# Kernel optimization log

Hardware: AMD Instinct MI355X
Metric: run time of the kernel (lower is better)

The kernel has to match this reference:

```python
import jax, jax.numpy as jnp
import numpy as np

B, C, H, T, K = 32, 128, 512, 8192, 512


def setup_inputs() -> dict:
    key = jax.random.key(0)
    ks = jax.random.split(key, 4)
    s = 0.02
    return {
        "x": jax.random.normal(ks[0], (B, C, T), dtype=jnp.float32),
        "up_w": jax.random.normal(ks[1], (H, C), dtype=jnp.float32) * s,
        "up_b": jnp.zeros((H,), jnp.float32),
        "sal_w": jax.random.normal(ks[2], (H, C), dtype=jnp.float32) * s,
        "sal_b": jnp.zeros((H,), jnp.float32),
        "down_w": jax.random.normal(ks[3], (C, H), dtype=jnp.float32) * s,
        "down_b": jnp.zeros((C,), jnp.float32),
        "k_sparse": K,
    }


def reference(x, up_w, up_b, sal_w, sal_b, down_w, down_b, k_sparse):
    b = x.shape[0]
    # 1x1 Conv1d == per-timestep GEMM
    sig = jnp.einsum('bct,hc->bht', x, up_w) + up_b[None, :, None]   # [B,H,T]
    sal = jnp.einsum('bct,hc->bht', x, sal_w) + sal_b[None, :, None]  # [B,H,T]
    # global softmax over flattened (H*T) per batch item
    flat = jax.nn.softmax(sal.reshape(b, -1), axis=-1)                # [B,H*T]
    # k-sparse: keep top-k values, zero everything else
    vals, idx = jax.lax.top_k(flat, k_sparse)                          # [B,K]
    sparse = jnp.zeros_like(flat).at[jnp.arange(b)[:, None], idx].set(vals)
    sal_sparse = sparse.reshape(sig.shape)                             # [B,H,T]
    gated = sig * sal_sparse                                           # [B,H,T]
    out = jnp.einsum('bht,ch->bct', gated, down_w) + down_b[None, :, None]
    return out
```

## Files before the change

### kernel.cpp

```cpp
#include <hip/hip_runtime.h>
#include <hip/hip_bf16.h>
#include <math.h>

#define BB 32
#define CC 128
#define HH 512
#define TT 8192
#define KMAX 512

#define NBIN 2048
#define CANDCAP 4096
#define HOTCAP 32768
#define TILES 2048
#define TLCAP 256
#define HFLOOR 0.6f
#define BW (0.875f / 2048.0f)
#define INVBW (2048.0f / 0.875f)
#define DELTA_C2 6e-3f
#define DELTA_C1 1.2e-2f

#define N_HIST 0
#define N_SUMEXP 262144
#define N_CANDCNT 262400
#define N_TILECNT 262528
#define N_ZERO 270720
#define N_TAU 270848
#define N_SELCNT 270976
#define N_CELLMAX 271360
#define N_TLIST 8659968
#define N_CANDVAL 10757120
#define N_CANDIDX 11805696
#define N_SELIDX 12329984
#define N_SELVAL 12395520
#define N_SWB 12461056
#define N_XF 12592128
#define N_DWT 79700992
#define N_NEED 79963136

#define O_HIST 0
#define O_SUMEXP 262144
#define O_CANDCNT 262400
#define O_HOTCNT 262528
#define O_ZERO 262656
#define O_TAU 262656
#define O_SELCNT 262784
#define O_CELLMAX 263168
#define O_HOTLIST 8651776
#define O_CANDVAL 8782848
#define O_CANDIDX 9831424
#define O_SELIDX 10355712
#define O_SELVAL 10421248

typedef __attribute__((ext_vector_type(8))) short short8;
typedef __attribute__((ext_vector_type(16))) float f32x16;
typedef __attribute__((address_space(3))) unsigned int lds_u32;
typedef const __attribute__((address_space(1))) unsigned int glb_u32;


__global__ void prep_w(const float* __restrict__ sw, short* __restrict__ swb) {
  int i = blockIdx.x * 256 + threadIdx.x;
  int m = i & 31, u = (i >> 5) & 1, kc = (i >> 6) & 7, w = (i >> 9) & 3, by = i >> 11;
  int h = by * 128 + w * 32 + m;
  int c0 = kc * 16 + u * 8;
  float4 f0 = *(const float4*)(sw + (size_t)h * CC + c0);
  float4 f1 = *(const float4*)(sw + (size_t)h * CC + c0 + 4);
  union { __hip_bfloat162 h2; unsigned u; } p0, p1, p2, p3;
  p0.h2 = __float22bfloat162_rn(make_float2(f0.x, f0.y));
  p1.h2 = __float22bfloat162_rn(make_float2(f0.z, f0.w));
  p2.h2 = __float22bfloat162_rn(make_float2(f1.x, f1.y));
  p3.h2 = __float22bfloat162_rn(make_float2(f1.z, f1.w));
  *(uint4*)(swb + (size_t)i * 8) = make_uint4(p0.u, p1.u, p2.u, p3.u);
}

__global__ void prep_dwt(const float* __restrict__ dw, float* __restrict__ dwt) {
  int i = blockIdx.x * 256 + threadIdx.x;
  int c = i & 127, h = i >> 7;
  dwt[(size_t)h * CC + c] = dw[(size_t)c * HH + h];
}

__global__ __launch_bounds__(256) void prep_xt(const float* __restrict__ x,
                                               short* __restrict__ xf) {
  __shared__ float Lt[128 * 128];
  int tid = threadIdx.x;
  int b = blockIdx.y, bx = blockIdx.x, t0g = bx * 128;
  const float* xb = x + (size_t)b * CC * TT;
  {
    int cq = tid >> 5, tq = tid & 31, t0 = tq * 4;
#pragma unroll
    for (int p = 0; p < 4; p++) {
      int c0 = p * 32 + cq * 4;
      float r0[4], r1[4], r2[4], r3[4];
      *(float4*)r0 = *(const float4*)(xb + (size_t)(c0 + 0) * TT + t0g + t0);
      *(float4*)r1 = *(const float4*)(xb + (size_t)(c0 + 1) * TT + t0g + t0);
      *(float4*)r2 = *(const float4*)(xb + (size_t)(c0 + 2) * TT + t0g + t0);
      *(float4*)r3 = *(const float4*)(xb + (size_t)(c0 + 3) * TT + t0g + t0);
#pragma unroll
      for (int j = 0; j < 4; j++) {
        int t = t0 + j;
        int addr = t * 128 + ((((c0 >> 2) ^ (t & 31)) << 2));
        *(float4*)&Lt[addr] = make_float4(r0[j], r1[j], r2[j], r3[j]);
      }
    }
  }
  __syncthreads();
  int u = tid & 1, m = (tid >> 1) & 31, nt = (tid >> 6) & 3;
  int t = nt * 32 + m;
  short* dst = xf + ((size_t)b * 64 + bx) * 16384 + nt * 4096 + u * 256 + m * 8;
#pragma unroll
  for (int kc = 0; kc < 8; kc++) {
    int c0 = kc * 16 + u * 8;
    float4 f0 = *(float4*)&Lt[t * 128 + ((((c0 >> 2) ^ (t & 31)) << 2))];
    float4 f1 = *(float4*)&Lt[t * 128 + (((((c0 + 4) >> 2) ^ (t & 31)) << 2))];
    union { __hip_bfloat162 h2; unsigned u; } p0, p1, p2, p3;
    p0.h2 = __float22bfloat162_rn(make_float2(f0.x, f0.y));
    p1.h2 = __float22bfloat162_rn(make_float2(f0.z, f0.w));
    p2.h2 = __float22bfloat162_rn(make_float2(f1.x, f1.y));
    p3.h2 = __float22bfloat162_rn(make_float2(f1.z, f1.w));
    *(uint4*)(dst + kc * 512) = make_uint4(p0.u, p1.u, p2.u, p3.u);
  }
}

__global__ __launch_bounds__(256) void pass_a_lds(const short* __restrict__ xf,
                                                  const short* __restrict__ swb,
                                                  const float* __restrict__ sb,
                                                  float* __restrict__ cellmax,
                                                  int* __restrict__ hist,
                                                  double* __restrict__ sumexp) {
  __shared__ short Xs[16384];
  __shared__ double sered[4];
  int tid = threadIdx.x;
  int w = tid >> 6, lane = tid & 63, m = lane & 31, u = lane >> 5;
  int id = blockIdx.x, b = blockIdx.y;
  int bx = ((id >> 5) << 3) | (id & 7);
  int by = (id >> 3) & 3;

  const short* xsl = xf + ((size_t)b * 64 + bx) * 16384;
  {
    const short* gs = xsl + w * 4096 + lane * 8;
    short* ls = &Xs[w * 4096];
#pragma unroll
    for (int i = 0; i < 8; i++) {
      __builtin_amdgcn_global_load_lds((glb_u32*)(gs + i * 512),
                                       (lds_u32*)(ls + i * 512), 16, 0, 0);
    }
  }

  const short* wb_ = swb + (size_t)(by * 4 + w) * 4096 + u * 256 + m * 8;
  short8 afr[8];
#pragma unroll
  for (int kc = 0; kc < 8; kc++) afr[kc] = *(const short8*)(wb_ + kc * 512);

  __syncthreads();

  f32x16 acc0, acc1, acc2, acc3;
#pragma unroll
  for (int r = 0; r < 16; r++) { acc0[r] = 0.f; acc1[r] = 0.f; acc2[r] = 0.f; acc3[r] = 0.f; }

  const short* xr = &Xs[u * 256 + m * 8];
#pragma unroll
  for (int kc = 0; kc < 8; kc++) {
    short8 b0 = *(const short8*)(xr + kc * 512);
    short8 b1 = *(const short8*)(xr + 4096 + kc * 512);
    short8 b2 = *(const short8*)(xr + 8192 + kc * 512);
    short8 b3 = *(const short8*)(xr + 12288 + kc * 512);
    acc0 = __builtin_amdgcn_mfma_f32_32x32x16_bf16(afr[kc], b0, acc0, 0, 0, 0);
    acc1 = __builtin_amdgcn_mfma_f32_32x32x16_bf16(afr[kc], b1, acc1, 0, 0, 0);
    acc2 = __builtin_amdgcn_mfma_f32_32x32x16_bf16(afr[kc], b2, acc2, 0, 0, 0);
    acc3 = __builtin_amdgcn_mfma_f32_32x32x16_bf16(afr[kc], b3, acc3, 0, 0, 0);
  }

  int h0 = by * 128;
  float tmax = -1e30f;
  float se = 0.f;
#define EPI(ACC)                                                              \
  {                                                                           \
    _Pragma("unroll") for (int g = 0; g < 4; g++) {                           \
      float bias4[4];                                                         \
      *(float4*)bias4 = *(const float4*)&sb[h0 + w * 32 + g * 8 + u * 4];     \
      _Pragma("unroll") for (int q = 0; q < 4; q++) {                         \
        float s = ACC[g * 4 + q] + bias4[q];                                  \
        tmax = fmaxf(tmax, s);                                                \
        se += __expf(s);                                                      \
        if (s >= HFLOOR) {                                                    \
          int bin = (int)((s - HFLOOR) * INVBW);                              \
          if (bin > NBIN - 1) bin = NBIN - 1;                                 \
          atomicAdd(&hist[b * NBIN + bin], 1);                                \
        }                                                                     \
      }                                                                       \
    }                                                                         \
  }
  EPI(acc0) EPI(acc1) EPI(acc2) EPI(acc3)
#undef EPI
  int cid = ((b * 4 + by) * 64 + bx) * 256 + tid;
  cellmax[cid] = tmax;
  double sed = (double)se;
#pragma unroll
  for (int mm = 1; mm < 64; mm <<= 1) sed += __shfl_xor(sed, mm);
  if (lane == 0) sered[w] = sed;
  __syncthreads();
  if (tid == 0) atomicAdd(&sumexp[b], sered[0] + sered[1] + sered[2] + sered[3]);
}

__global__ void pass_b(const int* __restrict__ hist, float* __restrict__ tau,
                       const int* __restrict__ kptr) {
  __shared__ int hsh[NBIN];
  __shared__ int ps[256];
  int b = blockIdx.x, tid = threadIdx.x;
  int part = 0;
#pragma unroll
  for (int j = 0; j < 8; j++) {
    int v = hist[b * NBIN + tid * 8 + j];
    hsh[tid * 8 + j] = v;
    part += v;
  }
  ps[tid] = part;
  __syncthreads();
  if (tid == 0) {
    int k = kptr[0];
    if (k < 1) k = 1;
    if (k > KMAX) k = KMAX;
    long cum = 0;
    float tv = HFLOOR;
    for (int i = 255; i >= 0; i--) {
      if (cum + ps[i] >= k) {
        long r = k - cum;
        long c2 = 0;
        for (int j = 7; j >= 0; j--) {
          c2 += hsh[i * 8 + j];
          if (c2 >= r) { tv = HFLOOR + (i * 8 + j) * BW; break; }
        }
        break;
      }
      cum += ps[i];
    }
    tau[b] = tv;
  }
}

__global__ void pass_c1_fast(const float* __restrict__ cellmax, const float* __restrict__ tau,
                             int* __restrict__ tilecnt, int* __restrict__ tlist) {
  int i = blockIdx.x * blockDim.x + threadIdx.x;
  float v = cellmax[i];
  int b = i >> 16;
  if (v >= tau[b] - DELTA_C1) {
    int tile = (b << 6) | ((i >> 8) & 63);
    int pos = atomicAdd(&tilecnt[tile], 1);
    if (pos < TLCAP) tlist[tile * TLCAP + pos] = i;
  }
}

__global__ __launch_bounds__(256) void pass_c2_fast(
    const float* __restrict__ x, const float* __restrict__ sw,
    const float* __restrict__ sb, const float* __restrict__ tau,
    const int* __restrict__ tilecnt, const int* __restrict__ tlist,
    int* __restrict__ candcnt, double* __restrict__ candval, int* __restrict__ candidx) {
  __shared__ float Xt[128 * 132];
  int tile = blockIdx.x;
  int b = tile >> 6, bx = tile & 63;
  int cnt = tilecnt[tile];
  if (cnt <= 0) return;
  if (cnt > TLCAP) cnt = TLCAP;
  int tid = threadIdx.x;
  {
    int cq = tid >> 5, tq = tid & 31;
    int t4 = tq * 4, snt = t4 >> 5, sa = (t4 >> 2) & 7;
    int sdst = snt * 32 + (((sa + snt) & 7) << 2);
    const float* xb = x + (size_t)b * CC * TT + bx * 128;
#pragma unroll
    for (int p = 0; p < 16; p++) {
      int c = p * 8 + cq;
      *(float4*)&Xt[c * 132 + sdst] = *(const float4*)(xb + (size_t)c * TT + t4);
    }
  }
  __syncthreads();
  int wv = tid >> 6, lane = tid & 63;
  float tmb = tau[b] - DELTA_C2;
  for (int s = wv; s < cnt; s += 4) {
    int cid = tlist[tile * TLCAP + s];
    int by = (cid >> 14) & 3;
    int ta = cid & 255;
    int w = ta >> 6, lc = ta & 63, m = lc & 31, u = lc >> 5;
    int nt = lane >> 4, r = lane & 15;
    int h = by * 128 + w * 32 + (r >> 2) * 8 + (r & 3) + 4 * u;
    int t = bx * 128 + nt * 32 + m;
    const float* swr = sw + (size_t)h * CC;
    int xoff = nt * 32 + (((((m >> 2) + nt) & 7)) << 2) + (m & 3);
    double a0 = 0.0, a1 = 0.0;
#pragma unroll 4
    for (int c = 0; c < CC; c += 2) {
      a0 = fma((double)Xt[c * 132 + xoff], (double)swr[c], a0);
      a1 = fma((double)Xt[(c + 1) * 132 + xoff], (double)swr[c + 1], a1);
    }
    double acc = a0 + a1 + (double)sb[h];
    if (acc >= (double)tmb) {
      int pos = atomicAdd(&candcnt[b], 1);
      if (pos < CANDCAP) {
        candval[b * CANDCAP + pos] = acc;
        candidx[b * CANDCAP + pos] = h * TT + t;
      }
    }
  }
}

__global__ void pass_d(const int* __restrict__ candcnt, const double* __restrict__ candval,
                       const int* __restrict__ candidx, const double* __restrict__ sumexp,
                       const int* __restrict__ kptr, int* __restrict__ selidx,
                       float* __restrict__ selval, int* __restrict__ selcnt) {
  __shared__ double sv[CANDCAP];
  __shared__ int si[CANDCAP];
  int b = blockIdx.x;
  int n = candcnt[b];
  if (n > CANDCAP) n = CANDCAP;
  int k = kptr[0];
  if (k < 0) k = 0;
  if (k > KMAX) k = KMAX;
  for (int i = threadIdx.x; i < n; i += blockDim.x) {
    sv[i] = candval[b * CANDCAP + i];
    si[i] = candidx[b * CANDCAP + i];
  }
  __syncthreads();
  double S = sumexp[b];
  for (int i = threadIdx.x; i < n; i += blockDim.x) {
    double vi = sv[i];
    int ii = si[i];
    int rank = 0;
    for (int q = 0; q < n; q++) {
      double vq = sv[q];
      rank += (vq > vi) || (vq == vi && si[q] < ii);
    }
    if (rank < k) {
      selidx[b * KMAX + rank] = ii;
      selval[b * KMAX + rank] = (float)(exp(vi) / S);
    }
  }
  if (threadIdx.x == 0) selcnt[b] = n < k ? n : k;
}

__global__ void pass_e1(const float* __restrict__ db, float* __restrict__ out) {
  int row = blockIdx.x;
  int c = row & (CC - 1);
  float v = db[c];
  float4 v4 = make_float4(v, v, v, v);
  float4* o = (float4*)(out + (size_t)row * TT);
#pragma unroll
  for (int q = 0; q < 8; q++) o[q * 256 + threadIdx.x] = v4;
}

__global__ void pass_e2_fast(const short* __restrict__ xf, const float* __restrict__ uw,
                             const float* __restrict__ ub, const float* __restrict__ dwt,
                             const int* __restrict__ selidx, const float* __restrict__ selval,
                             const int* __restrict__ selcnt, float* __restrict__ out) {
  int b = blockIdx.y, j = blockIdx.x;
  if (j >= selcnt[b]) return;
  int idx = selidx[b * KMAX + j];
  float val = selval[b * KMAX + j];
  int h = idx >> 13, t = idx & (TT - 1);
  int bx = t >> 7, tl = t & 127, nt = tl >> 5, m = tl & 31;
  int lane = threadIdx.x;
  const short* xt = xf + ((size_t)b * 64 + bx) * 16384 + nt * 4096 + m * 8;
  int off = (lane >> 3) * 512 + ((lane >> 2) & 1) * 256 + (lane & 3) * 2;
  __hip_bfloat162 hv = *(const __hip_bfloat162*)(xt + off);
  float2 xv = __bfloat1622float2(hv);
  int c0 = lane * 2;
  float2 wv = *(const float2*)(uw + (size_t)h * CC + c0);
  float p = xv.x * wv.x + xv.y * wv.y;
#pragma unroll
  for (int mm = 1; mm < 64; mm <<= 1) p += __shfl_xor(p, mm);
  float sig = p + ub[h];
  float g = sig * val;
  float2 dv = *(const float2*)(dwt + (size_t)h * CC + c0);
  atomicAdd(&out[((size_t)b * CC + c0) * TT + t], g * dv.x);
  atomicAdd(&out[((size_t)b * CC + c0 + 1) * TT + t], g * dv.y);
}

__global__ __launch_bounds__(256) void pass_a_slow(const float* __restrict__ x,
                                                   const float* __restrict__ sw,
                                                   const float* __restrict__ sb,
                                                   float* __restrict__ cellmax,
                                                   int* __restrict__ hist,
                                                   double* __restrict__ sumexp) {
  __shared__ short Ws[128 * 128];
  __shared__ short Xs[128 * 128];
  __shared__ float sbs[128];
  int tid = threadIdx.x;
  int b = blockIdx.z, by = blockIdx.y, bx = blockIdx.x;
  int h0 = by * 128, t0g = bx * 128;
  const float* xb = x + (size_t)b * CC * TT;
  {
    int cq = tid >> 5, tq = tid & 31;
    int t0 = tq * 4;
#pragma unroll
    for (int p = 0; p < 4; p++) {
      int c0 = p * 32 + cq * 4;
      float r0[4], r1[4], r2[4], r3[4];
      *(float4*)r0 = *(const float4*)(xb + (size_t)(c0 + 0) * TT + t0g + t0);
      *(float4*)r1 = *(const float4*)(xb + (size_t)(c0 + 1) * TT + t0g + t0);
      *(float4*)r2 = *(const float4*)(xb + (size_t)(c0 + 2) * TT + t0g + t0);
      *(float4*)r3 = *(const float4*)(xb + (size_t)(c0 + 3) * TT + t0g + t0);
#pragma unroll
      for (int j = 0; j < 4; j++) {
        int t = t0 + j;
        int addr = t * 128 + ((((c0 >> 3) ^ (t & 15)) << 3) | (c0 & 7));
        union { __hip_bfloat162 h; unsigned int u; } a0, a1;
        a0.h = __float22bfloat162_rn(make_float2(r0[j], r1[j]));
        a1.h = __float22bfloat162_rn(make_float2(r2[j], r3[j]));
        *(uint2*)&Xs[addr] = make_uint2(a0.u, a1.u);
      }
    }
  }
  {
    int hh = tid >> 1, c4 = (tid & 1) << 2;
#pragma unroll
    for (int k = 0; k < 16; k++) {
      int c0 = k * 8 + c4;
      float r[4];
      *(float4*)r = *(const float4*)(sw + (size_t)(h0 + hh) * CC + c0);
      int addr = hh * 128 + ((((c0 >> 3) ^ (hh & 15)) << 3) | (c0 & 7));
      union { __hip_bfloat162 h; unsigned int u; } a0, a1;
      a0.h = __float22bfloat162_rn(make_float2(r[0], r[1]));
      a1.h = __float22bfloat162_rn(make_float2(r[2], r[3]));
      *(uint2*)&Ws[addr] = make_uint2(a0.u, a1.u);
    }
  }
  if (tid < 128) sbs[tid] = sb[h0 + tid];
  __syncthreads();
  int w = tid >> 6, lane = tid & 63, m = lane & 31, u = lane >> 5;
  f32x16 acc0, acc1, acc2, acc3;
#pragma unroll
  for (int r = 0; r < 16; r++) { acc0[r] = 0.f; acc1[r] = 0.f; acc2[r] = 0.f; acc3[r] = 0.f; }
  const short* wrow = &Ws[(w * 32 + m) * 128];
  const short* xrow = &Xs[m * 128];
#pragma unroll
  for (int kc = 0; kc < 8; kc++) {
    int pc = ((((kc << 1) | u) ^ (m & 15)) << 3);
    short8 af = *(const short8*)(wrow + pc);
    short8 b0 = *(const short8*)(xrow + 0 * 32 * 128 + pc);
    short8 b1 = *(const short8*)(xrow + 1 * 32 * 128 + pc);
    short8 b2 = *(const short8*)(xrow + 2 * 32 * 128 + pc);
    short8 b3 = *(const short8*)(xrow + 3 * 32 * 128 + pc);
    acc0 = __builtin_amdgcn_mfma_f32_32x32x16_bf16(af, b0, acc0, 0, 0, 0);
    acc1 = __builtin_amdgcn_mfma_f32_32x32x16_bf16(af, b1, acc1, 0, 0, 0);
    acc2 = __builtin_amdgcn_mfma_f32_32x32x16_bf16(af, b2, acc2, 0, 0, 0);
    acc3 = __builtin_amdgcn_mfma_f32_32x32x16_bf16(af, b3, acc3, 0, 0, 0);
  }
  float tmax = -1e30f;
  float se = 0.f;
#define EPI(ACC)                                                              \
  {                                                                           \
    _Pragma("unroll") for (int g = 0; g < 4; g++) {                           \
      float bias4[4];                                                         \
      *(float4*)bias4 = *(float4*)&sbs[w * 32 + g * 8 + u * 4];               \
      _Pragma("unroll") for (int q = 0; q < 4; q++) {                         \
        float s = ACC[g * 4 + q] + bias4[q];                                  \
        tmax = fmaxf(tmax, s);                                                \
        se += __expf(s);                                                      \
        if (s >= HFLOOR) {                                                    \
          int bin = (int)((s - HFLOOR) * INVBW);                              \
          if (bin > NBIN - 1) bin = NBIN - 1;                                 \
          atomicAdd(&hist[b * NBIN + bin], 1);                                \
        }                                                                     \
      }                                                                       \
    }                                                                         \
  }
  EPI(acc0) EPI(acc1) EPI(acc2) EPI(acc3)
#undef EPI
  int cid = ((b * 4 + by) * 64 + bx) * 256 + tid;
  cellmax[cid] = tmax;
  double sed = (double)se;
#pragma unroll
  for (int mm = 1; mm < 64; mm <<= 1) sed += __shfl_xor(sed, mm);
  if ((tid & 63) == 0) atomicAdd(&sumexp[b], sed);
}

__global__ void pass_c1_slow(const float* __restrict__ cellmax, const float* __restrict__ tau,
                             int* __restrict__ hotcnt, int* __restrict__ hotlist) {
  int i = blockIdx.x * blockDim.x + threadIdx.x;
  float v = cellmax[i];
  int b = i >> 16;
  if (v >= tau[b] - DELTA_C1) {
    int pos = atomicAdd(hotcnt, 1);
    if (pos < HOTCAP) hotlist[pos] = i;
  }
}

__global__ void pass_c2_slow(const float* __restrict__ x, const float* __restrict__ sw,
                             const float* __restrict__ sb, const float* __restrict__ tau,
                             const int* __restrict__ hotcnt, const int* __restrict__ hotlist,
                             int* __restrict__ candcnt, double* __restrict__ candval,
                             int* __restrict__ candidx) {
  int j = blockIdx.x;
  int n = hotcnt[0];
  if (n > HOTCAP) n = HOTCAP;
  if (j >= n) return;
  int cid = hotlist[j];
  int b = cid >> 16, by = (cid >> 14) & 3, bx = (cid >> 8) & 63;
  int ta = cid & 255;
  int w = ta >> 6, lane = ta & 63, m = lane & 31, u = lane >> 5;
  int e = threadIdx.x;
  int nt = e >> 4, r = e & 15;
  int h = by * 128 + w * 32 + (r >> 2) * 8 + (r & 3) + 4 * u;
  int t = bx * 128 + nt * 32 + m;
  const float* xb = x + (size_t)b * CC * TT;
  double acc = 0.0;
#pragma unroll 8
  for (int c = 0; c < CC; c++)
    acc += (double)xb[(size_t)c * TT + t] * (double)sw[h * CC + c];
  acc += (double)sb[h];
  float tm = tau[b] - DELTA_C2;
  if (acc >= (double)tm) {
    int pos = atomicAdd(&candcnt[b], 1);
    if (pos < CANDCAP) {
      candval[b * CANDCAP + pos] = acc;
      candidx[b * CANDCAP + pos] = h * TT + t;
    }
  }
}

__global__ void pass_e2_slow(const float* __restrict__ x, const float* __restrict__ uw,
                             const float* __restrict__ ub, const float* __restrict__ dw,
                             const int* __restrict__ selidx, const float* __restrict__ selval,
                             const int* __restrict__ selcnt, float* __restrict__ out) {
  int b = blockIdx.y, j = blockIdx.x;
  if (j >= selcnt[b]) return;
  int idx = selidx[b * KMAX + j];
  float val = selval[b * KMAX + j];
  int h = idx >> 13, t = idx & (TT - 1);
  int c = threadIdx.x;
  const float* xb = x + (size_t)b * CC * TT;
  float p = xb[(size_t)c * TT + t] * uw[h * CC + c] +
            xb[(size_t)(c + 64) * TT + t] * uw[h * CC + c + 64];
#pragma unroll
  for (int m = 1; m < 64; m <<= 1) p += __shfl_xor(p, m);
  float sig = p + ub[h];
  float g = sig * val;
  atomicAdd(&out[((size_t)b * CC + c) * TT + t], g * dw[c * HH + h]);
  atomicAdd(&out[((size_t)b * CC + c + 64) * TT + t], g * dw[(c + 64) * HH + h]);
}

extern "C" void kernel_launch(void* const* d_in, const int* in_sizes, int n_in,
                              void* d_out, int out_size, void* d_ws, size_t ws_size,
                              hipStream_t stream) {
  const float* x = (const float*)d_in[0];
  const float* uw = (const float*)d_in[1];
  const float* ub = (const float*)d_in[2];
  const float* sw = (const float*)d_in[3];
  const float* sb = (const float*)d_in[4];
  const float* dw = (const float*)d_in[5];
  const float* db = (const float*)d_in[6];
  const int* kptr = (const int*)d_in[7];
  float* out = (float*)d_out;
  char* ws = (char*)d_ws;

  if (ws_size >= (size_t)N_NEED) {
    int* hist = (int*)(ws + N_HIST);
    double* sumexp = (double*)(ws + N_SUMEXP);
    int* candcnt = (int*)(ws + N_CANDCNT);
    int* tilecnt = (int*)(ws + N_TILECNT);
    float* tau = (float*)(ws + N_TAU);
    int* selcnt = (int*)(ws + N_SELCNT);
    float* cellmax = (float*)(ws + N_CELLMAX);
    int* tlist = (int*)(ws + N_TLIST);
    double* candval = (double*)(ws + N_CANDVAL);
    int* candidx = (int*)(ws + N_CANDIDX);
    int* selidx = (int*)(ws + N_SELIDX);
    float* selval = (float*)(ws + N_SELVAL);
    short* swb = (short*)(ws + N_SWB);
    short* xf = (short*)(ws + N_XF);
    float* dwt = (float*)(ws + N_DWT);

    (void)hipMemsetAsync(d_ws, 0, N_ZERO, stream);
    prep_w<<<32, 256, 0, stream>>>(sw, swb);
    prep_dwt<<<256, 256, 0, stream>>>(dw, dwt);
    prep_xt<<<dim3(64, 32), 256, 0, stream>>>(x, xf);
    pass_a_lds<<<dim3(256, 32), 256, 0, stream>>>(xf, swb, sb, cellmax, hist, sumexp);
    pass_b<<<32, 256, 0, stream>>>(hist, tau, kptr);
    pass_c1_fast<<<8192, 256, 0, stream>>>(cellmax, tau, tilecnt, tlist);
    pass_c2_fast<<<TILES, 256, 0, stream>>>(x, sw, sb, tau, tilecnt, tlist, candcnt,
                                            candval, candidx);
    pass_d<<<32, 256, 0, stream>>>(candcnt, candval, candidx, sumexp, kptr, selidx,
                                   selval, selcnt);
    pass_e1<<<BB * CC, 256, 0, stream>>>(db, out);
    pass_e2_fast<<<dim3(KMAX, BB), 64, 0, stream>>>(xf, uw, ub, dwt, selidx, selval,
                                                    selcnt, out);
  } else {
    int* hist = (int*)(ws + O_HIST);
    double* sumexp = (double*)(ws + O_SUMEXP);
    int* candcnt = (int*)(ws + O_CANDCNT);
    int* hotcnt = (int*)(ws + O_HOTCNT);
    float* tau = (float*)(ws + O_TAU);
    int* selcnt = (int*)(ws + O_SELCNT);
    float* cellmax = (float*)(ws + O_CELLMAX);
    int* hotlist = (int*)(ws + O_HOTLIST);
    double* candval = (double*)(ws + O_CANDVAL);
    int* candidx = (int*)(ws + O_CANDIDX);
    int* selidx = (int*)(ws + O_SELIDX);
    float* selval = (float*)(ws + O_SELVAL);

    (void)hipMemsetAsync(d_ws, 0, O_ZERO, stream);
    pass_a_slow<<<dim3(64, 4, 32), 256, 0, stream>>>(x, sw, sb, cellmax, hist, sumexp);
    pass_b<<<32, 256, 0, stream>>>(hist, tau, kptr);
    pass_c1_slow<<<8192, 256, 0, stream>>>(cellmax, tau, hotcnt, hotlist);
    pass_c2_slow<<<HOTCAP, 64, 0, stream>>>(x, sw, sb, tau, hotcnt, hotlist, candcnt,
                                            candval, candidx);
    pass_d<<<32, 256, 0, stream>>>(candcnt, candval, candidx, sumexp, kptr, selidx,
                                   selval, selcnt);
    pass_e1<<<BB * CC, 256, 0, stream>>>(db, out);
    pass_e2_slow<<<dim3(KMAX, BB), 64, 0, stream>>>(x, uw, ub, dw, selidx, selval,
                                                    selcnt, out);
  }
}
```

Measured before the change: 923.7 us.

## Transpose LDS tile in candidate rescoring kernel and use vectorized double-buffered loads

The candidate rescoring kernel now stores the x tile transposed in shared memory (time-major with XOR swizzle), so each lane reads contiguous float4 channel vectors instead of scalar strided values. Weight rows are read as float4 with a two-stage register double buffer, and the next candidate index is prefetched. Blocks double to 512 threads (8 waves) to process more candidates in parallel. The costs are scalar LDS stores during the transpose and higher register pressure from the buffers.

```diff
diff --git a/kernel.cpp b/kernel.cpp
--- a/kernel.cpp
+++ b/kernel.cpp
@@ -249,7 +249,7 @@
   }
 }
 
-__global__ __launch_bounds__(256) void pass_c2_fast(
+__global__ __launch_bounds__(512, 4) void pass_c2_fast(
     const float* __restrict__ x, const float* __restrict__ sw,
     const float* __restrict__ sb, const float* __restrict__ tau,
     const int* __restrict__ tilecnt, const int* __restrict__ tlist,
@@ -262,41 +262,71 @@
   if (cnt > TLCAP) cnt = TLCAP;
   int tid = threadIdx.x;
   {
-    int cq = tid >> 5, tq = tid & 31;
-    int t4 = tq * 4, snt = t4 >> 5, sa = (t4 >> 2) & 7;
-    int sdst = snt * 32 + (((sa + snt) & 7) << 2);
+    int cq = tid >> 5, tq = tid & 31, t4 = tq * 4;
     const float* xb = x + (size_t)b * CC * TT + bx * 128;
 #pragma unroll
-    for (int p = 0; p < 16; p++) {
-      int c = p * 8 + cq;
-      *(float4*)&Xt[c * 132 + sdst] = *(const float4*)(xb + (size_t)c * TT + t4);
+    for (int p = 0; p < 8; p++) {
+      int c = p * 16 + cq;
+      float4 v = *(const float4*)(xb + (size_t)c * TT + t4);
+      Xt[(t4 + 0) * 132 + (c ^ ((((t4 + 0) >> 2) & 7) << 2))] = v.x;
+      Xt[(t4 + 1) * 132 + (c ^ ((((t4 + 1) >> 2) & 7) << 2))] = v.y;
+      Xt[(t4 + 2) * 132 + (c ^ ((((t4 + 2) >> 2) & 7) << 2))] = v.z;
+      Xt[(t4 + 3) * 132 + (c ^ ((((t4 + 3) >> 2) & 7) << 2))] = v.w;
     }
   }
   __syncthreads();
   int wv = tid >> 6, lane = tid & 63;
   float tmb = tau[b] - DELTA_C2;
-  for (int s = wv; s < cnt; s += 4) {
-    int cid = tlist[tile * TLCAP + s];
-    int by = (cid >> 14) & 3;
-    int ta = cid & 255;
-    int w = ta >> 6, lc = ta & 63, m = lc & 31, u = lc >> 5;
-    int nt = lane >> 4, r = lane & 15;
-    int h = by * 128 + w * 32 + (r >> 2) * 8 + (r & 3) + 4 * u;
-    int t = bx * 128 + nt * 32 + m;
-    const float* swr = sw + (size_t)h * CC;
-    int xoff = nt * 32 + (((((m >> 2) + nt) & 7)) << 2) + (m & 3);
-    double a0 = 0.0, a1 = 0.0;
-#pragma unroll 4
-    for (int c = 0; c < CC; c += 2) {
-      a0 = fma((double)Xt[c * 132 + xoff], (double)swr[c], a0);
-      a1 = fma((double)Xt[(c + 1) * 132 + xoff], (double)swr[c + 1], a1);
-    }
-    double acc = a0 + a1 + (double)sb[h];
-    if (acc >= (double)tmb) {
-      int pos = atomicAdd(&candcnt[b], 1);
-      if (pos < CANDCAP) {
-        candval[b * CANDCAP + pos] = acc;
-        candidx[b * CANDCAP + pos] = h * TT + t;
+  if (wv >= cnt && wv >= 8) {}
+  int s = wv;
+  if (s < cnt) {
+    int cid_nxt = tlist[tile * TLCAP + s];
+    for (; s < cnt; s += 8) {
+      int cid = cid_nxt;
+      if (s + 8 < cnt) cid_nxt = tlist[tile * TLCAP + s + 8];
+      int by = (cid >> 14) & 3;
+      int ta = cid & 255;
+      int w = ta >> 6, lc = ta & 63, m = lc & 31, u = lc >> 5;
+      int nt = lane >> 4, r = lane & 15;
+      int h = by * 128 + w * 32 + (r >> 2) * 8 + (r & 3) + 4 * u;
+      int t = bx * 128 + nt * 32 + m;
+      float sbh = sb[h];
+      const float4* swr = (const float4*)(sw + (size_t)h * CC);
+      const float* xrow = &Xt[(nt * 32 + m) * 132];
+      int swz = ((m >> 2) & 7) << 2;
+      double acc0 = 0.0, acc1 = 0.0;
+      float4 wbuf[2][4], xbuf[2][4];
+#pragma unroll
+      for (int j = 0; j < 4; j++) {
+        wbuf[0][j] = swr[j];
+        xbuf[0][j] = *(const float4*)(xrow + ((j * 4) ^ swz));
+      }
+#pragma unroll
+      for (int ch = 0; ch < 8; ch++) {
+        int cur = ch & 1, nxt = cur ^ 1;
+        if (ch < 7) {
+#pragma unroll
+          for (int j = 0; j < 4; j++) {
+            wbuf[nxt][j] = swr[(ch + 1) * 4 + j];
+            xbuf[nxt][j] = *(const float4*)(xrow + (((ch + 1) * 16 + j * 4) ^ swz));
+          }
+        }
+#pragma unroll
+        for (int j = 0; j < 4; j++) {
+          float4 wvv = wbuf[cur][j], xvv = xbuf[cur][j];
+          acc0 = fma((double)xvv.x, (double)wvv.x, acc0);
+          acc1 = fma((double)xvv.y, (double)wvv.y, acc1);
+          acc0 = fma((double)xvv.z, (double)wvv.z, acc0);
+          acc1 = fma((double)xvv.w, (double)wvv.w, acc1);
+        }
+      }
+      double acc = acc0 + acc1 + (double)sbh;
+      if (acc >= (double)tmb) {
+        int pos = atomicAdd(&candcnt[b], 1);
+        if (pos < CANDCAP) {
+          candval[b * CANDCAP + pos] = acc;
+          candidx[b * CANDCAP + pos] = h * TT + t;
+        }
       }
     }
   }
@@ -575,7 +605,7 @@
     pass_a_lds<<<dim3(256, 32), 256, 0, stream>>>(xf, swb, sb, cellmax, hist, sumexp);
     pass_b<<<32, 256, 0, stream>>>(hist, tau, kptr);
     pass_c1_fast<<<8192, 256, 0, stream>>>(cellmax, tau, tilecnt, tlist);
-    pass_c2_fast<<<TILES, 256, 0, stream>>>(x, sw, sb, tau, tilecnt, tlist, candcnt,
+    pass_c2_fast<<<TILES, 512, 0, stream>>>(x, sw, sb, tau, tilecnt, tlist, candcnt,
                                             candval, candidx);
     pass_d<<<32, 256, 0, stream>>>(candcnt, candval, candidx, sumexp, kptr, selidx,
                                    selval, selcnt);
```

Result: no change. 930.9 us (+0.8%).

## Transpose LDS tile and software-pipeline candidate dot products in pass_c2

Applied to the files above, without the earlier changes.

Rewrites the exact-recompute pass so the x tile is stored transposed in LDS (time-major, XOR-swizzled on channels), letting each lane read float4 chunks along the channel dimension. The per-candidate FP64 dot product is split into four chunks with double-buffered register loads of weights and x, and the next candidate's index is prefetched and decoded while the current one finishes. Block size doubles to 512 threads (8 waves) so more candidates are processed per tile. This targets load latency and scalar LDS reads in pass_c2, at the cost of higher register pressure and a scattered transposing store into LDS.

```diff
diff --git a/kernel.cpp b/kernel.cpp
--- a/kernel.cpp
+++ b/kernel.cpp
@@ -249,7 +249,7 @@
   }
 }
 
-__global__ __launch_bounds__(256) void pass_c2_fast(
+__global__ __launch_bounds__(512, 2) void pass_c2_fast(
     const float* __restrict__ x, const float* __restrict__ sw,
     const float* __restrict__ sb, const float* __restrict__ tau,
     const int* __restrict__ tilecnt, const int* __restrict__ tlist,
@@ -262,44 +262,84 @@
   if (cnt > TLCAP) cnt = TLCAP;
   int tid = threadIdx.x;
   {
-    int cq = tid >> 5, tq = tid & 31;
-    int t4 = tq * 4, snt = t4 >> 5, sa = (t4 >> 2) & 7;
-    int sdst = snt * 32 + (((sa + snt) & 7) << 2);
+    int cq = tid >> 5, tq = tid & 31, t4 = tq * 4;
+    int sw4 = ((t4 >> 5) & 3) << 2;
     const float* xb = x + (size_t)b * CC * TT + bx * 128;
 #pragma unroll
-    for (int p = 0; p < 16; p++) {
-      int c = p * 8 + cq;
-      *(float4*)&Xt[c * 132 + sdst] = *(const float4*)(xb + (size_t)c * TT + t4);
+    for (int p = 0; p < 8; p++) {
+      int c = p * 16 + cq;
+      float4 v = *(const float4*)(xb + (size_t)c * TT + t4);
+      int cc = c ^ sw4;
+      Xt[(t4 + 0) * 132 + cc] = v.x;
+      Xt[(t4 + 1) * 132 + cc] = v.y;
+      Xt[(t4 + 2) * 132 + cc] = v.z;
+      Xt[(t4 + 3) * 132 + cc] = v.w;
     }
   }
   __syncthreads();
   int wv = tid >> 6, lane = tid & 63;
+  int nt = lane >> 4, r = lane & 15;
+  int swz = nt << 2;
   float tmb = tau[b] - DELTA_C2;
-  for (int s = wv; s < cnt; s += 4) {
-    int cid = tlist[tile * TLCAP + s];
-    int by = (cid >> 14) & 3;
-    int ta = cid & 255;
-    int w = ta >> 6, lc = ta & 63, m = lc & 31, u = lc >> 5;
-    int nt = lane >> 4, r = lane & 15;
-    int h = by * 128 + w * 32 + (r >> 2) * 8 + (r & 3) + 4 * u;
-    int t = bx * 128 + nt * 32 + m;
-    const float* swr = sw + (size_t)h * CC;
-    int xoff = nt * 32 + (((((m >> 2) + nt) & 7)) << 2) + (m & 3);
-    double a0 = 0.0, a1 = 0.0;
-#pragma unroll 4
-    for (int c = 0; c < CC; c += 2) {
-      a0 = fma((double)Xt[c * 132 + xoff], (double)swr[c], a0);
-      a1 = fma((double)Xt[(c + 1) * 132 + xoff], (double)swr[c + 1], a1);
-    }
-    double acc = a0 + a1 + (double)sb[h];
+  int tbase = tile * TLCAP;
+  if (wv >= cnt) return;
+
+#define DEC(CID)                                                        \
+  {                                                                     \
+    int by_ = ((CID) >> 14) & 3, ta_ = (CID) & 255;                     \
+    int w_ = ta_ >> 6, lc_ = ta_ & 63, m_ = lc_ & 31, u_ = lc_ >> 5;    \
+    h = by_ * 128 + w_ * 32 + (r >> 2) * 8 + (r & 3) + 4 * u_;          \
+    t = bx * 128 + nt * 32 + m_;                                        \
+    swp = (const float4*)(sw + (size_t)h * CC);                         \
+    xrp = &Xt[(nt * 32 + m_) * 132];                                    \
+    sbh = sb[h];                                                        \
+  }
+#define ISSUE(WB, XB, CH)                                               \
+  _Pragma("unroll") for (int j = 0; j < 8; j++) {                       \
+    WB[j] = swp[(CH) * 8 + j];                                          \
+    XB[j] = *(const float4*)(xrp + (((CH) * 32 + j * 4) ^ swz));        \
+  }
+#define DOT(WB, XB)                                                     \
+  _Pragma("unroll") for (int j = 0; j < 8; j++) {                       \
+    a0 = fma((double)XB[j].x, (double)WB[j].x, a0);                     \
+    a1 = fma((double)XB[j].y, (double)WB[j].y, a1);                     \
+    a2 = fma((double)XB[j].z, (double)WB[j].z, a2);                     \
+    a3 = fma((double)XB[j].w, (double)WB[j].w, a3);                     \
+  }
+
+  float4 wA[8], xA[8], wB[8], xB[8];
+  int h, t;
+  const float4* swp;
+  const float* xrp;
+  float sbh;
+  int s = wv;
+  int cid = tlist[tbase + s];
+  DEC(cid);
+  ISSUE(wA, xA, 0);
+  for (; s < cnt; ) {
+    int sn = s + 8;
+    int cidN = (sn < cnt) ? tlist[tbase + sn] : cid;
+    double a0 = 0.0, a1 = 0.0, a2 = 0.0, a3 = 0.0;
+    ISSUE(wB, xB, 1); DOT(wA, xA);
+    ISSUE(wA, xA, 2); DOT(wB, xB);
+    ISSUE(wB, xB, 3); DOT(wA, xA);
+    int hO = h, tO = t;
+    float sbO = sbh;
+    if (sn < cnt) { cid = cidN; DEC(cid); }
+    ISSUE(wA, xA, 0); DOT(wB, xB);
+    double acc = a0 + a1 + a2 + a3 + (double)sbO;
     if (acc >= (double)tmb) {
       int pos = atomicAdd(&candcnt[b], 1);
       if (pos < CANDCAP) {
         candval[b * CANDCAP + pos] = acc;
-        candidx[b * CANDCAP + pos] = h * TT + t;
+        candidx[b * CANDCAP + pos] = hO * TT + tO;
       }
     }
-  }
+    s = sn;
+  }
+#undef DEC
+#undef ISSUE
+#undef DOT
 }
 
 __global__ void pass_d(const int* __restrict__ candcnt, const double* __restrict__ candval,
@@ -575,7 +615,7 @@
     pass_a_lds<<<dim3(256, 32), 256, 0, stream>>>(xf, swb, sb, cellmax, hist, sumexp);
     pass_b<<<32, 256, 0, stream>>>(hist, tau, kptr);
     pass_c1_fast<<<8192, 256, 0, stream>>>(cellmax, tau, tilecnt, tlist);
-    pass_c2_fast<<<TILES, 256, 0, stream>>>(x, sw, sb, tau, tilecnt, tlist, candcnt,
+    pass_c2_fast<<<TILES, 512, 0, stream>>>(x, sw, sb, tau, tilecnt, tlist, candcnt,
                                             candval, candidx);
     pass_d<<<32, 256, 0, stream>>>(candcnt, candval, candidx, sumexp, kptr, selidx,
                                    selval, selcnt);
```

New measurement: 942.9 us. +2.1%, slower.

## Stage salience weights into LDS via async loads and widen candidate recompute blocks

Applied to the files above, without the earlier changes.

The candidate-recompute kernel now runs 512 threads (8 waves) per tile and transposes the x tile into LDS so each lane reads contiguous float4 channel vectors. Per candidate cell, each wave asynchronously loads the 16 needed weight rows into its own LDS slice with swizzled addressing, and the next candidate id is prefetched. This replaces strided global weight reads and scalar LDS reads in the double-precision dot product with vectorized LDS reads, at the cost of more LDS per block and a full vmcnt wait each iteration.

```diff
diff --git a/kernel.cpp b/kernel.cpp
--- a/kernel.cpp
+++ b/kernel.cpp
@@ -249,12 +249,13 @@
   }
 }
 
-__global__ __launch_bounds__(256) void pass_c2_fast(
+__global__ __launch_bounds__(512) void pass_c2_fast(
     const float* __restrict__ x, const float* __restrict__ sw,
     const float* __restrict__ sb, const float* __restrict__ tau,
     const int* __restrict__ tilecnt, const int* __restrict__ tlist,
     int* __restrict__ candcnt, double* __restrict__ candval, int* __restrict__ candidx) {
   __shared__ float Xt[128 * 132];
+  __shared__ float4 Wsh[8 * 512];
   int tile = blockIdx.x;
   int b = tile >> 6, bx = tile & 63;
   int cnt = tilecnt[tile];
@@ -262,36 +263,64 @@
   if (cnt > TLCAP) cnt = TLCAP;
   int tid = threadIdx.x;
   {
-    int cq = tid >> 5, tq = tid & 31;
-    int t4 = tq * 4, snt = t4 >> 5, sa = (t4 >> 2) & 7;
-    int sdst = snt * 32 + (((sa + snt) & 7) << 2);
+    int cq = tid >> 5, tq = tid & 31, t4 = tq * 4;
+    int sw4 = ((t4 >> 5) & 3) << 2;
     const float* xb = x + (size_t)b * CC * TT + bx * 128;
 #pragma unroll
-    for (int p = 0; p < 16; p++) {
-      int c = p * 8 + cq;
-      *(float4*)&Xt[c * 132 + sdst] = *(const float4*)(xb + (size_t)c * TT + t4);
+    for (int p = 0; p < 8; p++) {
+      int c = p * 16 + cq;
+      float4 v = *(const float4*)(xb + (size_t)c * TT + t4);
+      int cc = c ^ sw4;
+      Xt[(t4 + 0) * 132 + cc] = v.x;
+      Xt[(t4 + 1) * 132 + cc] = v.y;
+      Xt[(t4 + 2) * 132 + cc] = v.z;
+      Xt[(t4 + 3) * 132 + cc] = v.w;
     }
   }
   __syncthreads();
   int wv = tid >> 6, lane = tid & 63;
+  if (wv >= cnt) return;
+  int nt = lane >> 4, r = lane & 15;
+  int rs = r & 7;
+  int rowp = lane >> 5, colp = lane & 31;
   float tmb = tau[b] - DELTA_C2;
-  for (int s = wv; s < cnt; s += 4) {
-    int cid = tlist[tile * TLCAP + s];
-    int by = (cid >> 14) & 3;
-    int ta = cid & 255;
-    int w = ta >> 6, lc = ta & 63, m = lc & 31, u = lc >> 5;
-    int nt = lane >> 4, r = lane & 15;
-    int h = by * 128 + w * 32 + (r >> 2) * 8 + (r & 3) + 4 * u;
-    int t = bx * 128 + nt * 32 + m;
-    const float* swr = sw + (size_t)h * CC;
-    int xoff = nt * 32 + (((((m >> 2) + nt) & 7)) << 2) + (m & 3);
-    double a0 = 0.0, a1 = 0.0;
-#pragma unroll 4
-    for (int c = 0; c < CC; c += 2) {
-      a0 = fma((double)Xt[c * 132 + xoff], (double)swr[c], a0);
-      a1 = fma((double)Xt[(c + 1) * 132 + xoff], (double)swr[c + 1], a1);
-    }
-    double acc = a0 + a1 + (double)sb[h];
+  int tbase = tile * TLCAP;
+  float4* WbF4 = &Wsh[wv * 512];
+
+  int s = wv;
+  int cid = tlist[tbase + s];
+  for (; s < cnt;) {
+    int by_ = (cid >> 14) & 3, ta_ = cid & 255;
+    int w_ = ta_ >> 6, lc_ = ta_ & 63, m_ = lc_ & 31, u_ = lc_ >> 5;
+    int hbase = by_ * 128 + w_ * 32 + 4 * u_;
+    int h = hbase + (r >> 2) * 8 + (r & 3);
+    int t = bx * 128 + nt * 32 + m_;
+    const float* xrp = &Xt[(nt * 32 + m_) * 132];
+#pragma unroll
+    for (int i = 0; i < 8; i++) {
+      int row_ = i * 2 + rowp;
+      int h_ = hbase + ((row_ >> 2) << 3) + (row_ & 3);
+      int c4 = colp ^ (row_ & 7);
+      __builtin_amdgcn_global_load_lds(
+          (glb_u32*)(sw + (size_t)h_ * CC + c4 * 4),
+          (lds_u32*)((char*)WbF4 + i * 1024), 16, 0, 0);
+    }
+    float sbh = sb[h];
+    int sn = s + 8;
+    int cidN = (sn < cnt) ? tlist[tbase + sn] : 0;
+    asm volatile("s_waitcnt vmcnt(0)" ::: "memory");
+    __builtin_amdgcn_sched_barrier(0);
+    double a0 = 0.0, a1 = 0.0, a2 = 0.0, a3 = 0.0;
+#pragma unroll
+    for (int j = 0; j < 32; j++) {
+      float4 w4 = WbF4[r * 32 + (j ^ rs)];
+      float4 x4 = *(const float4*)(xrp + ((j * 4) ^ (nt * 4)));
+      a0 = fma((double)x4.x, (double)w4.x, a0);
+      a1 = fma((double)x4.y, (double)w4.y, a1);
+      a2 = fma((double)x4.z, (double)w4.z, a2);
+      a3 = fma((double)x4.w, (double)w4.w, a3);
+    }
+    double acc = a0 + a1 + a2 + a3 + (double)sbh;
     if (acc >= (double)tmb) {
       int pos = atomicAdd(&candcnt[b], 1);
       if (pos < CANDCAP) {
@@ -299,6 +328,8 @@
         candidx[b * CANDCAP + pos] = h * TT + t;
       }
     }
+    s = sn;
+    cid = cidN;
   }
 }
 
@@ -575,7 +606,7 @@
     pass_a_lds<<<dim3(256, 32), 256, 0, stream>>>(xf, swb, sb, cellmax, hist, sumexp);
     pass_b<<<32, 256, 0, stream>>>(hist, tau, kptr);
     pass_c1_fast<<<8192, 256, 0, stream>>>(cellmax, tau, tilecnt, tlist);
-    pass_c2_fast<<<TILES, 256, 0, stream>>>(x, sw, sb, tau, tilecnt, tlist, candcnt,
+    pass_c2_fast<<<TILES, 512, 0, stream>>>(x, sw, sb, tau, tilecnt, tlist, candcnt,
                                             candval, candidx);
     pass_d<<<32, 256, 0, stream>>>(candcnt, candval, candidx, sumexp, kptr, selidx,
                                    selval, selcnt);
```

New measurement: 923.1 us. No clear change (-0.1%).
